# Kernel tuning notes

Measured on AMD Instinct MI355X. Metric: run time of the kernel, lower is better.

Reference implementation:

```python
import jax, jax.numpy as jnp
import numpy as np

N = 20000      # nodes
E = 320000     # edges (avg degree 16)
DIN = 50       # PPI input features
C = 121        # PPI classes
HID = 1024     # 4 heads x 256 concatenated
H3 = 6         # heads in last layer


def setup_inputs() -> dict:
    key = jax.random.key(0)
    ks = jax.random.split(key, 7)
    X = jax.random.normal(ks[0], (N, DIN), jnp.float32)
    edge_index = jax.random.randint(ks[1], (2, E), 0, N, dtype=jnp.int32)
    def w(k, i, o):
        return jax.random.normal(k, (i, o), jnp.float32) / jnp.sqrt(jnp.float32(i))
    return {
        "X": X,
        "edge_index": edge_index,
        "W1": w(ks[2], DIN, HID),        # 4 heads x 256, concatenated
        "W2": w(ks[3], HID, HID),        # 4 heads x 256 GCN weights
        "S2": w(ks[4], HID, HID),        # 4 heads x 256 skip linears
        "W3": w(ks[5], HID, H3 * C),     # 6 heads x num_classes GCN weights
        "S3": w(ks[6], HID, H3 * C),     # 6 heads x num_classes skip linears
    }


def _agg(xw, row, col, norm, n):
    # GCN symmetric-normalized neighbor sum: out[col] += norm * xw[row]
    return jax.ops.segment_sum(xw[row] * norm[:, None], col, num_segments=n)


def reference(X, edge_index, W1, W2, S2, W3, S3):
    n = X.shape[0]
    row, col = edge_index[0], edge_index[1]
    # degree at targets (add_self_loops=False), D^{-1/2} A D^{-1/2} normalization
    deg = jax.ops.segment_sum(jnp.ones(row.shape, X.dtype), col, num_segments=n)
    dis = jnp.where(deg > 0, deg ** -0.5, 0.0)
    norm = dis[row] * dis[col]
    # layer 1: 4 GCN heads (weights concatenated), elu, concat
    h1 = jax.nn.elu(_agg(X @ W1, row, col, norm, n))              # [N, 1024]
    # layer 2: 4 GCN heads + linear skip, elu, concat
    h2 = jax.nn.elu(_agg(h1 @ W2, row, col, norm, n) + h1 @ S2)   # [N, 1024]
    # layer 3: 6 GCN heads + linear skip, average over heads (Identity act)
    y = _agg(h2 @ W3, row, col, norm, n) + h2 @ S3                # [N, 6*C]
    return y.reshape(n, H3, C).mean(axis=1)                       # [N, C]
```

## Files before the change

### kernel.cpp

```cpp
#include <hip/hip_runtime.h>
#include <hip/hip_bf16.h>
#include <math.h>

#define N_NODES 20000
#define N_EDGES 320000
#define DIN 50
#define HID 1024
#define NC3 726
#define NCLS 121
#define KCAT 2048
#define NQ 242

typedef __attribute__((ext_vector_type(8))) _Float16 half8;
typedef __attribute__((ext_vector_type(4))) float floatx4;

__device__ __forceinline__ unsigned short f2h(float v) {
    _Float16 h = (_Float16)v;
    return __builtin_bit_cast(unsigned short, h);
}
__device__ __forceinline__ float h2f(unsigned short u) {
    return (float)__builtin_bit_cast(_Float16, u);
}

__device__ __forceinline__ void async16(const void* g, void* l) {
    __builtin_amdgcn_global_load_lds(
        (const __attribute__((address_space(1))) void*)g,
        (__attribute__((address_space(3))) void*)l,
        16, 0, 0);
}


__global__ void zero_int_kernel(int* p, int n) {
    int i = blockIdx.x * blockDim.x + threadIdx.x;
    if (i < n) p[i] = 0;
}

__global__ __launch_bounds__(1024) void scan_kernel(const int* __restrict__ deg,
                                                    int* __restrict__ offs,
                                                    int* __restrict__ cursor,
                                                    float* __restrict__ dis,
                                                    int n, int total) {
    __shared__ int part[1024];
    int t = threadIdx.x;
    const int CH = (n + 1023) / 1024;
    int base0 = t * CH;
    int s = 0;
    for (int i = 0; i < CH; ++i) {
        int idx = base0 + i;
        if (idx < n) s += deg[idx];
    }
    part[t] = s;
    __syncthreads();
    for (int d = 1; d < 1024; d <<= 1) {
        int v = (t >= d) ? part[t - d] : 0;
        __syncthreads();
        part[t] += v;
        __syncthreads();
    }
    int run = part[t] - s;
    for (int i = 0; i < CH; ++i) {
        int idx = base0 + i;
        if (idx < n) {
            int d = deg[idx];
            offs[idx] = run;
            cursor[idx] = run;
            dis[idx] = d > 0 ? rsqrtf((float)d) : 0.0f;
            run += d;
        }
    }
    if (t == 1023) offs[n] = total;
}

__global__ void scatter_kernel(const int* __restrict__ row, const int* __restrict__ col,
                               const float* __restrict__ dis, int* __restrict__ cursor,
                               int* __restrict__ csr_src, float* __restrict__ csr_w, int e) {
    int i = blockIdx.x * blockDim.x + threadIdx.x;
    if (i < e) {
        int r = row[i], c = col[i];
        float nm = dis[r] * dis[c];
        int pos = atomicAdd(&cursor[c], 1);
        csr_src[pos] = r;
        csr_w[pos] = nm;
    }
}

__global__ __launch_bounds__(256) void prep_kernel(const int* __restrict__ ecol,
                                                   int* __restrict__ deg,
                                                   const float* __restrict__ W1,
                                                   unsigned short* __restrict__ Bt1,
                                                   const float* __restrict__ W2,
                                                   const float* __restrict__ S2,
                                                   unsigned short* __restrict__ Bt2,
                                                   const float* __restrict__ W3,
                                                   const float* __restrict__ S3,
                                                   unsigned short* __restrict__ Bt3) {
    __shared__ unsigned short tile[32][33];
    const int b = blockIdx.x;
    const int tid = threadIdx.x;

    if (b < 2048) {
        int src = b >> 10;
        int t = b & 1023;
        int k0 = (t >> 5) * 32;
        int n0 = (t & 31) * 32;
        const float* W = src ? S2 : W2;
        int koff = src ? HID : 0;
        int tx = tid & 31;
        int ty = tid >> 5;
#pragma unroll
        for (int r = 0; r < 32; r += 8)
            tile[ty + r][tx] = f2h(W[(size_t)(k0 + ty + r) * HID + n0 + tx]);
        __syncthreads();
#pragma unroll
        for (int r = 0; r < 32; r += 8)
            Bt2[(size_t)(n0 + ty + r) * KCAT + koff + k0 + tx] = tile[tx][ty + r];
    } else if (b < 2304) {
        int tb = b - 2048;
        int src = tb >> 7;
        int t = tb & 127;
        int k0 = (t >> 2) * 32;
        int c0 = (t & 3) * 32;
        const float* W = src ? S3 : W3;
        int tx = tid & 31;
        int ty = tid >> 5;
#pragma unroll
        for (int r = 0; r < 32; r += 8) {
            int k = k0 + ty + r, c = c0 + tx;
            float v = 0.0f;
            if (c < NCLS) {
                const float* p = W + (size_t)k * NC3 + c;
                v = (p[0] + p[121] + p[242] + p[363] + p[484] + p[605]) * (1.0f / 6.0f);
            }
            tile[ty + r][tx] = f2h(v);
        }
        __syncthreads();
#pragma unroll
        for (int r = 0; r < 32; r += 8) {
            int c = c0 + ty + r;
            if (c < NCLS)
                Bt3[(size_t)(src * NCLS + c) * HID + k0 + tx] = tile[tx][ty + r];
        }
    } else if (b < 2560) {
        int i = (b - 2304) * 256 + tid;
        int n = i / 64, k = i - n * 64;
        Bt1[i] = (k < DIN) ? f2h(W1[(size_t)k * HID + n]) : (unsigned short)0;
    } else {
        int i = (b - 2560) * 256 + tid;
        if (i < N_EDGES) atomicAdd(&deg[ecol[i]], 1);
    }
}


__global__ __launch_bounds__(64) void aggX_kernel(const float* __restrict__ X,
                                                  const int* __restrict__ offs,
                                                  const int* __restrict__ csr_src,
                                                  const float* __restrict__ csr_w,
                                                  unsigned short* __restrict__ gX) {
    int n = blockIdx.x;
    int t = threadIdx.x;
    float a = 0.0f;
    if (t < DIN) {
        int p0 = offs[n], p1 = offs[n + 1];
        for (int p = p0; p < p1; ++p) {
            a = fmaf(csr_w[p], X[(size_t)csr_src[p] * DIN + t], a);
        }
    }
    gX[(size_t)n * 64 + t] = (t < DIN) ? f2h(a) : (unsigned short)0;
}

__global__ __launch_bounds__(256) void agg_slice_kernel(const unsigned short* __restrict__ h,
                                                        const int* __restrict__ offs,
                                                        const int* __restrict__ csr_src,
                                                        const float* __restrict__ csr_w,
                                                        unsigned short* __restrict__ g) {
    const int f = blockIdx.x;
    const int slice = f & 7;
    const int nb = f >> 3;
    const int tid = threadIdx.x;
    const int n = nb * 16 + (tid >> 4);
    const int coloff = slice * 128 + (tid & 15) * 8;
    const unsigned short* hp = h + coloff;

    float a[8] = {0, 0, 0, 0, 0, 0, 0, 0};
    int p0 = offs[n], p1 = offs[n + 1];
    for (int p = p0; p < p1; ++p) {
        int s = csr_src[p];
        float w = csr_w[p];
        uint4 v = *(const uint4*)&hp[(size_t)s * HID];
        const unsigned short* vs = (const unsigned short*)&v;
#pragma unroll
        for (int j = 0; j < 8; ++j) a[j] = fmaf(w, h2f(vs[j]), a[j]);
    }
    unsigned short ov[8];
#pragma unroll
    for (int j = 0; j < 8; ++j) ov[j] = f2h(a[j]);
    *(uint4*)&g[(size_t)n * HID + coloff] = *(const uint4*)ov;
}

__global__ __launch_bounds__(256) void agg3_kernel(const unsigned short* __restrict__ Q,
                                                   const int* __restrict__ offs,
                                                   const int* __restrict__ csr_src,
                                                   const float* __restrict__ csr_w,
                                                   float* __restrict__ out) {
    int n = blockIdx.x * 2 + (threadIdx.x >> 7);
    int c = threadIdx.x & 127;
    if (c >= NCLS) return;
    float a = 0.0f;
    int p0 = offs[n], p1 = offs[n + 1];
    for (int p = p0; p < p1; ++p) {
        a = fmaf(csr_w[p], h2f(Q[(size_t)csr_src[p] * NQ + c]), a);
    }
    a += h2f(Q[(size_t)n * NQ + NCLS + c]);
    out[(size_t)n * NCLS + c] = a;
}


#define GBM 128
#define GBN 128
#define GBK 32

template <int EPI>
__global__ __launch_bounds__(256, 4) void mfma_gemm_kernel(
        const unsigned short* __restrict__ Ag, const unsigned short* __restrict__ Ah,
        const unsigned short* __restrict__ Bt,
        void* __restrict__ Co,
        int M, int N, int ldc, int ktot, int khalf, int kw,
        int NB, int MB, int mchunk) {
    __shared__ __align__(16) unsigned short sA[2][GBM * GBK];
    __shared__ __align__(16) unsigned short sB[2][GBN * GBK];

    const int f = blockIdx.x;
    const int xcd = f & 7;
    const int r0 = f >> 3;
    const int nB = r0 % NB;
    const int mi = r0 / NB;
    const int mB = xcd * mchunk + mi;
    if (mB >= MB) return;
    const int bm = mB * GBM;
    const int bn = nB * GBN;
    const int ks = blockIdx.y;

    const int tid = threadIdx.x;
    const int lane = tid & 63;
    const int wave = tid >> 6;
    const int wm = wave >> 1;
    const int wn = wave & 1;

    const int st_r = tid >> 2;
    const int st_slot = tid & 3;
    const int st_c = (st_slot ^ ((st_r >> 1) & 3)) * 8;
    const int st_lds = st_r * GBK + st_slot * 8;

    int agm[2], bgn[2];
#pragma unroll
    for (int p = 0; p < 2; ++p) {
        int gm = bm + st_r + p * 64;
        agm[p] = gm < M ? gm : M - 1;
        int gn = bn + st_r + p * 64;
        bgn[p] = gn < N ? gn : N - 1;
    }

    const int frow = lane & 15;
    const int fkc = (((lane >> 4) ^ ((frow >> 1) & 3))) * 8;

    floatx4 acc[4][4];
#pragma unroll
    for (int i = 0; i < 4; ++i)
#pragma unroll
        for (int j = 0; j < 4; ++j) acc[i][j] = (floatx4){0.f, 0.f, 0.f, 0.f};

    auto issue = [&](int k0, int buf) {
        const unsigned short* ap = (k0 < khalf) ? Ag : Ah;
        int ka = (k0 < khalf) ? k0 : k0 - khalf;
#pragma unroll
        for (int p = 0; p < 2; ++p) {
            async16(&ap[(size_t)agm[p] * khalf + ka + st_c],
                    &sA[buf][p * 64 * GBK + st_lds]);
            async16(&Bt[(size_t)bgn[p] * ktot + k0 + st_c],
                    &sB[buf][p * 64 * GBK + st_lds]);
        }
    };

    const int tw = kw / GBK;
    const int t0 = ks * tw;
    const int t1 = t0 + tw;

    issue(t0 * GBK, 0);

    for (int t = t0; t < t1; ++t) {
        __syncthreads();
        if (t + 1 < t1) issue((t + 1) * GBK, (t + 1) & 1);

        const unsigned short* a_base = sA[t & 1];
        const unsigned short* b_base = sB[t & 1];
        half8 fa[4], fb[4];
#pragma unroll
        for (int i = 0; i < 4; ++i)
            fa[i] = *(const half8*)&a_base[(wm * 64 + i * 16 + frow) * GBK + fkc];
#pragma unroll
        for (int j = 0; j < 4; ++j)
            fb[j] = *(const half8*)&b_base[(wn * 64 + j * 16 + frow) * GBK + fkc];
#pragma unroll
        for (int i = 0; i < 4; ++i)
#pragma unroll
            for (int j = 0; j < 4; ++j)
                acc[i][j] = __builtin_amdgcn_mfma_f32_16x16x32_f16(fa[i], fb[j], acc[i][j], 0, 0, 0);
    }

    const int c_r0 = (lane >> 4) * 4;
    const int c_c = lane & 15;
#pragma unroll
    for (int i = 0; i < 4; ++i)
#pragma unroll
        for (int j = 0; j < 4; ++j) {
            int gn = bn + wn * 64 + j * 16 + c_c;
            if (gn >= N) continue;
#pragma unroll
            for (int r = 0; r < 4; ++r) {
                int gm = bm + wm * 64 + i * 16 + c_r0 + r;
                if (gm >= M) continue;
                float v = acc[i][j][r];
                if (EPI == 0) {
                    v = v > 0 ? v : expf(v) - 1.0f;
                    ((unsigned short*)Co)[(size_t)gm * ldc + gn] = f2h(v);
                } else if (EPI == 1) {
                    atomicAdd(&((float*)Co)[(size_t)gm * ldc + gn], v);
                } else {
                    ((unsigned short*)Co)[(size_t)gm * ldc + gn] = f2h(v);
                }
            }
        }
}


static inline size_t align_up(size_t x, size_t a) { return (x + a - 1) & ~(a - 1); }

extern "C" void kernel_launch(void* const* d_in, const int* in_sizes, int n_in,
                              void* d_out, int out_size, void* d_ws, size_t ws_size,
                              hipStream_t stream) {
    const float* X  = (const float*)d_in[0];
    const int* erow = (const int*)d_in[1];
    const int* ecol = (const int*)d_in[1] + N_EDGES;
    const float* W1 = (const float*)d_in[2];
    const float* W2 = (const float*)d_in[3];
    const float* S2 = (const float*)d_in[4];
    const float* W3 = (const float*)d_in[5];
    const float* S3 = (const float*)d_in[6];
    float* out = (float*)d_out;

    char* w = (char*)d_ws;
    int* deg     = (int*)w;             w += align_up((size_t)N_NODES * 4, 256);
    int* offs    = (int*)w;             w += align_up((size_t)(N_NODES + 1) * 4, 256);
    int* cursor  = (int*)w;             w += align_up((size_t)N_NODES * 4, 256);
    int* csr_src = (int*)w;             w += align_up((size_t)N_EDGES * 4, 256);
    float* dis   = (float*)w;           w += align_up((size_t)N_NODES * 4, 256);
    float* csr_w = (float*)w;           w += align_up((size_t)N_EDGES * 4, 256);
    unsigned short* gXh = (unsigned short*)w; w += align_up((size_t)N_NODES * 64 * 2, 256);
    unsigned short* h1 = (unsigned short*)w;  w += align_up((size_t)N_NODES * HID * 2, 256);
    unsigned short* g  = (unsigned short*)w;  w += align_up((size_t)N_NODES * HID * 2, 256);
    unsigned short* h2 = (unsigned short*)w;  w += align_up((size_t)N_NODES * HID * 2, 256);
    unsigned short* Qh = (unsigned short*)w;  w += align_up((size_t)N_NODES * NQ * 2, 256);
    unsigned short* Bt1 = (unsigned short*)w; w += align_up((size_t)HID * 64 * 2, 256);
    unsigned short* Bt2 = (unsigned short*)w; w += align_up((size_t)HID * KCAT * 2, 256);
    unsigned short* Bt3 = (unsigned short*)w; w += align_up((size_t)NQ * HID * 2, 256);

    const int TB = 256;
    int nb_n = (N_NODES + TB - 1) / TB;

    zero_int_kernel<<<nb_n, TB, 0, stream>>>(deg, N_NODES);
    prep_kernel<<<3810, 256, 0, stream>>>(ecol, deg, W1, Bt1, W2, S2, Bt2, W3, S3, Bt3);

    scan_kernel<<<1, 1024, 0, stream>>>(deg, offs, cursor, dis, N_NODES, N_EDGES);
    scatter_kernel<<<(N_EDGES + TB - 1) / TB, TB, 0, stream>>>(erow, ecol, dis, cursor,
                                                               csr_src, csr_w, N_EDGES);

    const int MB = (N_NODES + GBM - 1) / GBM;
    const int mchunk = (MB + 7) / 8;
    const int NB2 = HID / GBN;
    const int NB3 = (NQ + GBN - 1) / GBN;
    const int AGG_GRID = 8 * (N_NODES / 16);

    aggX_kernel<<<N_NODES, 64, 0, stream>>>(X, offs, csr_src, csr_w, gXh);
    mfma_gemm_kernel<0><<<dim3(8 * mchunk * NB2, 1), 256, 0, stream>>>(
        gXh, gXh, Bt1, h1, N_NODES, HID, HID, 64, 64, 64, NB2, MB, mchunk);

    agg_slice_kernel<<<AGG_GRID, 256, 0, stream>>>(h1, offs, csr_src, csr_w, g);
    mfma_gemm_kernel<0><<<dim3(8 * mchunk * NB2, 1), 256, 0, stream>>>(
        g, h1, Bt2, h2, N_NODES, HID, HID, KCAT, HID, KCAT, NB2, MB, mchunk);

    mfma_gemm_kernel<2><<<dim3(8 * mchunk * NB3, 1), 256, 0, stream>>>(
        h2, h2, Bt3, Qh, N_NODES, NQ, NQ, HID, HID, HID, NB3, MB, mchunk);
    agg3_kernel<<<N_NODES / 2, 256, 0, stream>>>(Qh, offs, csr_src, csr_w, out);
}
```

Baseline: 485.1 us.

## Add 256x256 ping-pong pipelined GEMM kernel for layer-2 concatenated matmul

```diff
diff --git a/kernel.cpp b/kernel.cpp
--- a/kernel.cpp
+++ b/kernel.cpp
@@ -328,6 +328,176 @@
                 } else {
                     ((unsigned short*)Co)[(size_t)gm * ldc + gn] = f2h(v);
                 }
+            }
+        }
+}
+
+
+#define BM8 256
+#define BN8 256
+#define BK8 64
+
+__global__ __launch_bounds__(512, 2) void gemm8p_kernel(
+        const unsigned short* __restrict__ Ag, const unsigned short* __restrict__ Ah,
+        const unsigned short* __restrict__ Bt,
+        unsigned short* __restrict__ Co,
+        int M, int N, int ldc, int ktot, int khalf, int NBn) {
+    __shared__ __align__(16) unsigned short sA[2][BM8 * BK8];
+    __shared__ __align__(16) unsigned short sB[2][BN8 * BK8];
+
+    const int nwg = gridDim.x;
+    const int orig = blockIdx.x;
+    const int q = nwg >> 3, r = nwg & 7;
+    const int xcd = orig & 7;
+    const int wg = (xcd < r ? xcd * (q + 1) : r * (q + 1) + (xcd - r) * q) + (orig >> 3);
+    const int mB = wg / NBn;
+    const int nB = wg - mB * NBn;
+    const int bm = mB * BM8;
+    const int bn = nB * BN8;
+
+    const int tid = threadIdx.x;
+    const int lane = tid & 63;
+    const int wave = tid >> 6;
+    const int wm = wave >> 2;
+    const int wn = wave & 3;
+
+    const int srow = tid >> 3;
+    const int sslot = tid & 7;
+    const int swcol = (sslot ^ (srow & 7)) * 8;
+    const int ldso = srow * BK8 + sslot * 8;
+
+    size_t aoff[4], boff[4];
+#pragma unroll
+    for (int rr = 0; rr < 4; ++rr) {
+        int gm = bm + rr * 64 + srow; if (gm >= M) gm = M - 1;
+        aoff[rr] = (size_t)gm * khalf + swcol;
+        int gn = bn + rr * 64 + srow; if (gn >= N) gn = N - 1;
+        boff[rr] = (size_t)gn * ktot + swcol;
+    }
+
+    auto stage_b = [&](int t, int h) {
+        const int k0 = t * BK8;
+        unsigned short* dst = sB[t & 1];
+        async16(Bt + boff[2 * h] + k0,     dst + (2 * h) * 64 * BK8 + ldso);
+        async16(Bt + boff[2 * h + 1] + k0, dst + (2 * h + 1) * 64 * BK8 + ldso);
+    };
+    auto stage_a = [&](int t, int w) {
+        const int k0 = t * BK8;
+        const unsigned short* ap = (k0 < khalf) ? Ag : Ah;
+        const int ka = (k0 < khalf) ? k0 : k0 - khalf;
+        unsigned short* dst = sA[t & 1];
+        async16(ap + aoff[w] + ka,     dst + w * 64 * BK8 + ldso);
+        async16(ap + aoff[w + 2] + ka, dst + (w + 2) * 64 * BK8 + ldso);
+    };
+
+    floatx4 acc[8][4];
+#pragma unroll
+    for (int i = 0; i < 8; ++i)
+#pragma unroll
+        for (int j = 0; j < 4; ++j) acc[i][j] = (floatx4){0.f, 0.f, 0.f, 0.f};
+
+    const int NT = ktot / BK8;
+    const int frow = lane & 15;
+    const int fgrp = lane >> 4;
+    const int coff0 = ((fgrp)     ^ (frow & 7)) * 8;
+    const int coff1 = ((4 + fgrp) ^ (frow & 7)) * 8;
+
+    stage_b(0, 0); stage_b(0, 1); stage_a(0, 0); stage_a(0, 1);
+    asm volatile("s_waitcnt vmcnt(2)" ::: "memory");
+    __builtin_amdgcn_s_barrier();
+
+    for (int t = 0; t < NT; ++t) {
+        const unsigned short* ab = sA[t & 1];
+        const unsigned short* bb = sB[t & 1];
+        const bool pf = (t + 1 < NT);
+        half8 fa[4][2], fb[4][2];
+
+#pragma unroll
+        for (int j = 0; j < 4; ++j) {
+            fb[j][0] = *(const half8*)&bb[(wn * 64 + j * 16 + frow) * BK8 + coff0];
+            fb[j][1] = *(const half8*)&bb[(wn * 64 + j * 16 + frow) * BK8 + coff1];
+        }
+#pragma unroll
+        for (int i = 0; i < 4; ++i) {
+            fa[i][0] = *(const half8*)&ab[(wm * 128 + i * 16 + frow) * BK8 + coff0];
+            fa[i][1] = *(const half8*)&ab[(wm * 128 + i * 16 + frow) * BK8 + coff1];
+        }
+        if (pf) stage_b(t + 1, 0);
+        __builtin_amdgcn_s_barrier();
+        __builtin_amdgcn_s_setprio(1);
+#pragma unroll
+        for (int kk = 0; kk < 2; ++kk)
+#pragma unroll
+            for (int i = 0; i < 4; ++i)
+#pragma unroll
+                for (int j = 0; j < 2; ++j)
+                    acc[i][j] = __builtin_amdgcn_mfma_f32_16x16x32_f16(fa[i][kk], fb[j][kk], acc[i][j], 0, 0, 0);
+        __builtin_amdgcn_s_setprio(0);
+        __builtin_amdgcn_s_barrier();
+
+        if (pf) stage_b(t + 1, 1);
+        __builtin_amdgcn_s_barrier();
+        __builtin_amdgcn_s_setprio(1);
+#pragma unroll
+        for (int kk = 0; kk < 2; ++kk)
+#pragma unroll
+            for (int i = 0; i < 4; ++i)
+#pragma unroll
+                for (int j = 2; j < 4; ++j)
+                    acc[i][j] = __builtin_amdgcn_mfma_f32_16x16x32_f16(fa[i][kk], fb[j][kk], acc[i][j], 0, 0, 0);
+        __builtin_amdgcn_s_setprio(0);
+        if (pf) { asm volatile("s_waitcnt vmcnt(4)" ::: "memory"); }
+        else    { asm volatile("s_waitcnt vmcnt(0)" ::: "memory"); }
+        __builtin_amdgcn_s_barrier();
+
+#pragma unroll
+        for (int i = 0; i < 4; ++i) {
+            fa[i][0] = *(const half8*)&ab[(wm * 128 + 64 + i * 16 + frow) * BK8 + coff0];
+            fa[i][1] = *(const half8*)&ab[(wm * 128 + 64 + i * 16 + frow) * BK8 + coff1];
+        }
+        if (pf) stage_a(t + 1, 0);
+        __builtin_amdgcn_s_barrier();
+        __builtin_amdgcn_s_setprio(1);
+#pragma unroll
+        for (int kk = 0; kk < 2; ++kk)
+#pragma unroll
+            for (int i = 0; i < 4; ++i)
+#pragma unroll
+                for (int j = 2; j < 4; ++j)
+                    acc[4 + i][j] = __builtin_amdgcn_mfma_f32_16x16x32_f16(fa[i][kk], fb[j][kk], acc[4 + i][j], 0, 0, 0);
+        __builtin_amdgcn_s_setprio(0);
+        __builtin_amdgcn_s_barrier();
+
+        if (pf) stage_a(t + 1, 1);
+        __builtin_amdgcn_s_barrier();
+        __builtin_amdgcn_s_setprio(1);
+#pragma unroll
+        for (int kk = 0; kk < 2; ++kk)
+#pragma unroll
+            for (int i = 0; i < 4; ++i)
+#pragma unroll
+                for (int j = 0; j < 2; ++j)
+                    acc[4 + i][j] = __builtin_amdgcn_mfma_f32_16x16x32_f16(fa[i][kk], fb[j][kk], acc[4 + i][j], 0, 0, 0);
+        __builtin_amdgcn_s_setprio(0);
+        if (pf) { asm volatile("s_waitcnt vmcnt(2)" ::: "memory"); }
+        __builtin_amdgcn_s_barrier();
+    }
+
+    const int c_c = lane & 15;
+    const int c_r0 = fgrp * 4;
+#pragma unroll
+    for (int i = 0; i < 8; ++i)
+#pragma unroll
+        for (int j = 0; j < 4; ++j) {
+            const int gn = bn + wn * 64 + j * 16 + c_c;
+            if (gn >= N) continue;
+#pragma unroll
+            for (int rr = 0; rr < 4; ++rr) {
+                const int gm = bm + wm * 128 + i * 16 + c_r0 + rr;
+                if (gm >= M) continue;
+                float v = acc[i][j][rr];
+                v = v > 0 ? v : expf(v) - 1.0f;
+                Co[(size_t)gm * ldc + gn] = f2h(v);
             }
         }
 }
@@ -380,13 +550,16 @@
     const int NB3 = (NQ + GBN - 1) / GBN;
     const int AGG_GRID = 8 * (N_NODES / 16);
 
+    const int MB8 = (N_NODES + BM8 - 1) / BM8;
+    const int NB8 = HID / BN8;
+
     aggX_kernel<<<N_NODES, 64, 0, stream>>>(X, offs, csr_src, csr_w, gXh);
     mfma_gemm_kernel<0><<<dim3(8 * mchunk * NB2, 1), 256, 0, stream>>>(
         gXh, gXh, Bt1, h1, N_NODES, HID, HID, 64, 64, 64, NB2, MB, mchunk);
 
     agg_slice_kernel<<<AGG_GRID, 256, 0, stream>>>(h1, offs, csr_src, csr_w, g);
-    mfma_gemm_kernel<0><<<dim3(8 * mchunk * NB2, 1), 256, 0, stream>>>(
-        g, h1, Bt2, h2, N_NODES, HID, HID, KCAT, HID, KCAT, NB2, MB, mchunk);
+    gemm8p_kernel<<<dim3(MB8 * NB8), 512, 0, stream>>>(
+        g, h1, Bt2, h2, N_NODES, HID, HID, KCAT, HID, NB8);
 
     mfma_gemm_kernel<2><<<dim3(8 * mchunk * NB3, 1), 256, 0, stream>>>(
         h2, h2, Bt3, Qh, N_NODES, NQ, NQ, HID, HID, HID, NB3, MB, mchunk);
```

Measured after the change: 504.3 us. +3.9%, slower.
